# Kernel optimization log

Measured on AMD Instinct MI355X. Metric: run time of the kernel, lower is better.

Reference implementation:

```python
import jax, jax.numpy as jnp
import numpy as np

B, NV, RN, SN = 1, 4, 1024, 128
H = W = 256
C_FEAT = 32   # img_feat_dim
D_VIEW = 32   # view transformer d_model
PE_D = 8      # PE_d_hid
D_RAY = D_VIEW + PE_D  # 40
NHEAD = 8
EPS_LN = 1e-5


def _layernorm(x, g, b):
    m = x.mean(-1, keepdims=True)
    v = ((x - m) ** 2).mean(-1, keepdims=True)
    return (x - m) * jax.lax.rsqrt(v + EPS_LN) * g + b


def _linear_attention(q, k, v):
    # LoFTR kernelized linear attention; q,k,v: (n, L, h, d)
    Q = jax.nn.elu(q) + 1.0
    K = jax.nn.elu(k) + 1.0
    L = v.shape[1]
    KV = jnp.einsum('nshd,nshv->nhdv', K, v / L)
    Z = 1.0 / (jnp.einsum('nlhd,nhd->nlh', Q, K.sum(axis=1)) + 1e-6)
    return jnp.einsum('nlhd,nhdv,nlh->nlhv', Q, KV, Z) * L


def _loftr_self_layer(x, Wq, Wk, Wv, Wm, g1, b1, W1, W2, g2, b2):
    # LoFTREncoderLayer with self-attention (x is both query and source)
    n, L, d = x.shape
    dim = d // NHEAD
    q = (x @ Wq).reshape(n, L, NHEAD, dim)
    k = (x @ Wk).reshape(n, L, NHEAD, dim)
    v = (x @ Wv).reshape(n, L, NHEAD, dim)
    msg = _linear_attention(q, k, v).reshape(n, L, d) @ Wm
    msg = _layernorm(msg, g1, b1)
    msg = jax.nn.relu(jnp.concatenate([x, msg], -1) @ W1) @ W2
    msg = _layernorm(msg, g2, b2)
    return x + msg


def _grid_sample_2d(img, pix):
    # img: (N,C,H,W); pix: (N,RN,SN,2) in pixel coords.
    # bilinear, align_corners=True, zero padding; mask = in-bounds.
    N, C, Hh, Ww = img.shape
    x, y = pix[..., 0], pix[..., 1]
    mask = ((x >= 0) & (x <= Ww - 1) & (y >= 0) & (y <= Hh - 1)).astype(img.dtype)
    x0 = jnp.floor(x)
    y0 = jnp.floor(y)
    flat = img.reshape(N, C, Hh * Ww)

    def gather(ix, iy):
        valid = ((ix >= 0) & (ix < Ww) & (iy >= 0) & (iy < Hh)).astype(img.dtype)
        idx = (jnp.clip(iy, 0, Hh - 1) * Ww + jnp.clip(ix, 0, Ww - 1)).astype(jnp.int32)
        out = jnp.take_along_axis(flat, idx.reshape(N, 1, -1), axis=2)
        return out.reshape(N, C, ix.shape[1], ix.shape[2]) * valid[:, None]

    wx1 = x - x0
    wy1 = y - y0
    out = (gather(x0, y0) * ((1 - wx1) * (1 - wy1))[:, None]
           + gather(x0 + 1, y0) * (wx1 * (1 - wy1))[:, None]
           + gather(x0, y0 + 1) * ((1 - wx1) * wy1)[:, None]
           + gather(x0 + 1, y0 + 1) * (wx1 * wy1)[:, None])
    return out, mask


def _order_posenc(d_hid, n):
    pos = np.arange(n)[:, None].astype(np.float64)
    j = np.arange(d_hid)[None, :]
    tab = pos / np.power(10000.0, 2 * (j // 2) / d_hid)
    tab[:, 0::2] = np.sin(tab[:, 0::2])
    tab[:, 1::2] = np.cos(tab[:, 1::2])
    return jnp.asarray(tab, dtype=jnp.float32)


def _forward(point3D, source_imgs, source_imgs_feat, ref_pose_inv, source_poses_inv,
             source_poses, view_token,
             vt_Wq, vt_Wk, vt_Wv, vt_Wm, vt_g1, vt_b1, vt_W1, vt_W2, vt_g2, vt_b2,
             rt_Wq, rt_Wk, rt_Wv, rt_Wm, rt_g1, rt_b1, rt_W1, rt_W2, rt_g2, rt_b2,
             dm_W1, dm_b1, dm_W2, dm_b2, dm_W3, dm_b3,
             rw_W1, rw_b1, rw_W2, rw_b2, rw_W3, rw_b3):
    b, nv, _, h, w = source_imgs.shape
    _, rn, sn, _ = point3D.shape

    # relative viewing directions (B,NV,RN,SN,3)
    v1 = point3D - ref_pose_inv[:, None, None, :3, -1]
    v2 = point3D[:, None] - source_poses_inv[:, :, None, None, :3, -1]
    v1 = v1 / jnp.linalg.norm(v1, axis=-1, keepdims=True)
    v2 = v2 / jnp.linalg.norm(v2, axis=-1, keepdims=True)
    dir_relative = v1[:, None] - v2

    # project points into all source views: (B,NV,3,RN,SN)
    pts_h = jnp.concatenate([point3D, jnp.ones_like(point3D[..., :1])], -1)
    pip = jnp.einsum('bnij,brsj->bnirs', source_poses, pts_h)[:, :, :3]
    mask_valid_depth = (pip[:, :, 2] > 0).astype(point3D.dtype)
    pix = pip[:, :, :2] / pip[:, :, 2:3]
    grid = jnp.moveaxis(pix, 2, -1).reshape(b * nv, rn, sn, 2)

    feat_s, mask = _grid_sample_2d(source_imgs_feat.reshape(b * nv, -1, h, w), grid)
    rgb_s, _ = _grid_sample_2d(source_imgs.reshape(b * nv, -1, h, w), grid)
    mask = mask.reshape(b, nv, rn, sn) * mask_valid_depth

    # per-point multi-view tokens: (B*RN*SN, NV, C)
    x = feat_s.reshape(b, nv, -1, rn, sn).transpose(0, 3, 4, 1, 2).reshape(b * rn * sn, nv, -1)
    tok = jnp.broadcast_to(view_token, (x.shape[0], 1, view_token.shape[-1]))
    x = jnp.concatenate([tok, x], axis=1)  # prepend view token -> L = NV+1
    x = _loftr_self_layer(x, vt_Wq, vt_Wk, vt_Wv, vt_Wm, vt_g1, vt_b1, vt_W1, vt_W2, vt_g2, vt_b2)

    x1 = jnp.moveaxis(x, 1, 0)          # (NV+1, B*RN*SN, C)
    view_feature = x1[1:]
    x = x1[0].reshape(b * rn, sn, -1)   # token output per sample along ray

    pe = _order_posenc(PE_D, sn)        # (SN, 8)
    x = jnp.concatenate([x, jnp.broadcast_to(pe, (b * rn, sn, PE_D))], -1)
    x = _loftr_self_layer(x, rt_Wq, rt_Wk, rt_Wv, rt_Wm, rt_g1, rt_b1, rt_W1, rt_W2, rt_g2, rt_b2)

    hdm = jax.nn.relu(x @ dm_W1 + dm_b1)
    hdm = jax.nn.relu(hdm @ dm_W2 + dm_b2)
    srdf = hdm @ dm_W3 + dm_b3           # (B*RN, SN, 1)

    # radiance blending weights over views
    vf = view_feature.reshape(nv, b, rn, sn, -1).transpose(1, 2, 3, 0, 4)  # (B,RN,SN,NV,C)
    dr = dir_relative.transpose(0, 2, 3, 1, 4)                             # (B,RN,SN,NV,3)
    xw = jnp.concatenate([vf, dr], -1)
    xw = jax.nn.relu(xw @ rw_W1 + rw_b1)
    xw = jax.nn.relu(xw @ rw_W2 + rw_b2)
    xw = xw @ rw_W3 + rw_b3                                                # (B,RN,SN,NV,1)
    m = mask.transpose(0, 2, 3, 1)[..., None]
    xw = jnp.where(m == 0, -1e9, xw)
    weight = jax.nn.softmax(xw, axis=-2)
    w_bn = weight[..., 0].transpose(0, 3, 1, 2)[:, :, None]                # (B,NV,1,RN,SN)
    radiance = (rgb_s.reshape(b, nv, 3, rn, sn) * w_bn).sum(axis=1)        # (B,3,RN,SN)
    radiance = radiance.transpose(0, 2, 3, 1).reshape(b * rn * sn, 3)
    return radiance, srdf, pip


def setup_inputs() -> dict:
    key = jax.random.key(0)
    ks = jax.random.split(key, 4)
    u = jax.random.uniform(ks[0], (B, RN, SN, 3), dtype=jnp.float32)
    point3D = jnp.concatenate([u[..., :2] - 0.5, u[..., 2:] + 1.0], -1)  # x,y in [-.5,.5], z in [1,2]
    source_imgs = jax.random.normal(ks[1], (B, NV, 3, H, W), dtype=jnp.float32) * 0.5
    source_imgs_feat = jax.random.normal(ks[2], (B, NV, C_FEAT, H, W), dtype=jnp.float32) * 0.5

    f = 200.0
    P = np.array([[f, 0, W / 2, 0], [0, f, H / 2, 0], [0, 0, 1, 0], [0, 0, 0, 1]], np.float32)
    source_poses = jnp.asarray(np.broadcast_to(P, (B, NV, 4, 4)).copy())
    ref_pose_inv = jnp.asarray(np.broadcast_to(np.eye(4, dtype=np.float32), (B, 4, 4)).copy())
    spi = np.broadcast_to(np.eye(4, dtype=np.float32), (B, NV, 4, 4)).copy()
    spi[:, :, 0, 3] = np.linspace(-0.2, 0.2, NV, dtype=np.float32)  # camera centers
    source_poses_inv = jnp.asarray(spi)

    pk = jax.random.split(ks[3], 20)

    def lin(k, i, o):
        return jax.random.normal(k, (i, o), dtype=jnp.float32) * 0.05

    d, dr = D_VIEW, D_RAY
    params = dict(
        view_token=jax.random.normal(pk[0], (1, d), dtype=jnp.float32),
        vt_Wq=lin(pk[1], d, d), vt_Wk=lin(pk[2], d, d), vt_Wv=lin(pk[3], d, d), vt_Wm=lin(pk[4], d, d),
        vt_g1=jnp.ones(d), vt_b1=jnp.zeros(d),
        vt_W1=lin(pk[5], 2 * d, 2 * d), vt_W2=lin(pk[6], 2 * d, d),
        vt_g2=jnp.ones(d), vt_b2=jnp.zeros(d),
        rt_Wq=lin(pk[7], dr, dr), rt_Wk=lin(pk[8], dr, dr), rt_Wv=lin(pk[9], dr, dr), rt_Wm=lin(pk[10], dr, dr),
        rt_g1=jnp.ones(dr), rt_b1=jnp.zeros(dr),
        rt_W1=lin(pk[11], 2 * dr, 2 * dr), rt_W2=lin(pk[12], 2 * dr, dr),
        rt_g2=jnp.ones(dr), rt_b2=jnp.zeros(dr),
        dm_W1=lin(pk[13], dr, 32), dm_b1=jnp.zeros(32),
        dm_W2=lin(pk[14], 32, 16), dm_b2=jnp.zeros(16),
        dm_W3=lin(pk[15], 16, 1), dm_b3=jnp.zeros(1),
        rw_W1=lin(pk[16], d + 3, 16), rw_b1=jnp.zeros(16),
        rw_W2=lin(pk[17], 16, 8), rw_b2=jnp.zeros(8),
        rw_W3=lin(pk[18], 8, 1), rw_b3=jnp.zeros(1),
    )
    out = dict(point3D=point3D, source_imgs=source_imgs, source_imgs_feat=source_imgs_feat,
               ref_pose_inv=ref_pose_inv, source_poses_inv=source_poses_inv,
               source_poses=source_poses)
    out.update(params)
    return out


def reference(point3D, source_imgs, source_imgs_feat, ref_pose_inv, source_poses_inv,
              source_poses, view_token,
              vt_Wq, vt_Wk, vt_Wv, vt_Wm, vt_g1, vt_b1, vt_W1, vt_W2, vt_g2, vt_b2,
              rt_Wq, rt_Wk, rt_Wv, rt_Wm, rt_g1, rt_b1, rt_W1, rt_W2, rt_g2, rt_b2,
              dm_W1, dm_b1, dm_W2, dm_b2, dm_W3, dm_b3,
              rw_W1, rw_b1, rw_W2, rw_b2, rw_W3, rw_b3):
    return _forward(point3D, source_imgs, source_imgs_feat, ref_pose_inv, source_poses_inv,
                    source_poses, view_token,
                    vt_Wq, vt_Wk, vt_Wv, vt_Wm, vt_g1, vt_b1, vt_W1, vt_W2, vt_g2, vt_b2,
                    rt_Wq, rt_Wk, rt_Wv, rt_Wm, rt_g1, rt_b1, rt_W1, rt_W2, rt_g2, rt_b2,
                    dm_W1, dm_b1, dm_W2, dm_b2, dm_W3, dm_b3,
                    rw_W1, rw_b1, rw_W2, rw_b2, rw_W3, rw_b3)
```

## Files before the change

kernel.cpp:

```cpp
#include <hip/hip_runtime.h>
#include <math.h>

#define NPTS   131072
#define NVIEW  4
#define IMH    256
#define IMW    256

#define WS_FEATT   0u
#define WS_IMGT    8388608u
#define WS_X1      9437184u
#define WS_XR      26214400u
#define WS_MSG     31457280u
#define WS_RGB     36700160u
#define WS_DIR     38273024u
#define WS_MASK    39845888u

__device__ __forceinline__ float elup1(float t) { return t > 0.f ? t + 1.f : expf(t); }

__global__ __launch_bounds__(256) void k0_transpose(
    const float* __restrict__ feat, const float* __restrict__ img,
    float* __restrict__ featT, float* __restrict__ imgT)
{
    int tid = blockIdx.x * 256 + threadIdx.x;
    int v = tid >> 16, pix = tid & 65535;
    float buf[32];
#pragma unroll
    for (int c = 0; c < 32; ++c)
        buf[c] = feat[((size_t)(v * 32 + c) << 16) + pix];
    float4* dst = (float4*)(featT + ((size_t)tid << 5));
#pragma unroll
    for (int q = 0; q < 8; ++q)
        dst[q] = make_float4(buf[4*q], buf[4*q+1], buf[4*q+2], buf[4*q+3]);
    float4 rgb;
    rgb.x = img[((size_t)(v * 3 + 0) << 16) + pix];
    rgb.y = img[((size_t)(v * 3 + 1) << 16) + pix];
    rgb.z = img[((size_t)(v * 3 + 2) << 16) + pix];
    rgb.w = 0.f;
    *(float4*)(imgT + ((size_t)tid << 2)) = rgb;
}

__global__ __launch_bounds__(256) void k1_geom_sample(
    const float* __restrict__ p3d, const float* __restrict__ rpi,
    const float* __restrict__ spi, const float* __restrict__ sp,
    const float* __restrict__ featT, const float* __restrict__ imgT,
    float* __restrict__ x1, float* __restrict__ rgbw,
    float* __restrict__ dirw, float* __restrict__ maskw,
    float* __restrict__ outpip)
{
    int tid = blockIdx.x * 256 + threadIdx.x;
    int p = tid >> 2, v = tid & 3;
    float X = p3d[p * 3 + 0], Y = p3d[p * 3 + 1], Z = p3d[p * 3 + 2];

    float a0 = X - rpi[3], a1 = Y - rpi[7], a2 = Z - rpi[11];
    float na = sqrtf(a0 * a0 + a1 * a1 + a2 * a2);
    a0 /= na; a1 /= na; a2 /= na;
    const float* sv = spi + v * 16;
    float b0 = X - sv[3], b1 = Y - sv[7], b2 = Z - sv[11];
    float nb = sqrtf(b0 * b0 + b1 * b1 + b2 * b2);
    b0 /= nb; b1 /= nb; b2 /= nb;
    dirw[(size_t)p * 12 + v * 3 + 0] = a0 - b0;
    dirw[(size_t)p * 12 + v * 3 + 1] = a1 - b1;
    dirw[(size_t)p * 12 + v * 3 + 2] = a2 - b2;

    const float* P = sp + v * 16;
    float pip0 = P[0] * X + P[1] * Y + P[2]  * Z + P[3];
    float pip1 = P[4] * X + P[5] * Y + P[6]  * Z + P[7];
    float pip2 = P[8] * X + P[9] * Y + P[10] * Z + P[11];
    outpip[(size_t)(v * 3 + 0) * NPTS + p] = pip0;
    outpip[(size_t)(v * 3 + 1) * NPTS + p] = pip1;
    outpip[(size_t)(v * 3 + 2) * NPTS + p] = pip2;

    float gx = pip0 / pip2, gy = pip1 / pip2;
    float inb = (gx >= 0.f && gx <= 255.f && gy >= 0.f && gy <= 255.f) ? 1.f : 0.f;
    float mvd = pip2 > 0.f ? 1.f : 0.f;
    maskw[(size_t)p * 4 + v] = inb * mvd;

    float x0f = floorf(gx), y0f = floorf(gy);
    float wx = gx - x0f, wy = gy - y0f;
    int ix0 = (int)x0f, iy0 = (int)y0f;
    float tw[4] = { (1.f-wx)*(1.f-wy), wx*(1.f-wy), (1.f-wx)*wy, wx*wy };
    int tdx[4] = { 0, 1, 0, 1 };
    int tdy[4] = { 0, 0, 1, 1 };

    float facc[32];
#pragma unroll
    for (int c = 0; c < 32; ++c) facc[c] = 0.f;
    float r0 = 0.f, r1 = 0.f, r2 = 0.f;

#pragma unroll
    for (int tno = 0; tno < 4; ++tno) {
        int ix = ix0 + tdx[tno], iy = iy0 + tdy[tno];
        float valid = (ix >= 0 && ix < IMW && iy >= 0 && iy < IMH) ? 1.f : 0.f;
        int cx = min(max(ix, 0), IMW - 1), cy = min(max(iy, 0), IMH - 1);
        float wgt = tw[tno] * valid;
        size_t base = ((size_t)v << 16) + ((size_t)cy << 8) + (size_t)cx;
        const float4* fp = (const float4*)(featT + base * 32);
#pragma unroll
        for (int q = 0; q < 8; ++q) {
            float4 f4 = fp[q];
            facc[4*q+0] += f4.x * wgt; facc[4*q+1] += f4.y * wgt;
            facc[4*q+2] += f4.z * wgt; facc[4*q+3] += f4.w * wgt;
        }
        float4 rp = *(const float4*)(imgT + base * 4);
        r0 += rp.x * wgt; r1 += rp.y * wgt; r2 += rp.z * wgt;
    }

    float4* xd = (float4*)(x1 + ((size_t)p * 4 + v) * 32);
#pragma unroll
    for (int q = 0; q < 8; ++q)
        xd[q] = make_float4(facc[4*q], facc[4*q+1], facc[4*q+2], facc[4*q+3]);
    rgbw[(size_t)p * 12 + v * 3 + 0] = r0;
    rgbw[(size_t)p * 12 + v * 3 + 1] = r1;
    rgbw[(size_t)p * 12 + v * 3 + 2] = r2;
}

#define K2_BLK    128
#define K2_PTS    24
#define K2_GRID   1024
#define K2_NGRP   ((NPTS + K2_PTS - 1) / K2_PTS)

__device__ __forceinline__ void fma4(const float4 xv, const float* __restrict__ w,
                                     const int stride, float* __restrict__ acc)
{
#pragma unroll
    for (int j = 0; j < 32; ++j) acc[j] = fmaf(xv.x, w[j],            acc[j]);
#pragma unroll
    for (int j = 0; j < 32; ++j) acc[j] = fmaf(xv.y, w[stride + j],   acc[j]);
#pragma unroll
    for (int j = 0; j < 32; ++j) acc[j] = fmaf(xv.z, w[2*stride + j], acc[j]);
#pragma unroll
    for (int j = 0; j < 32; ++j) acc[j] = fmaf(xv.w, w[3*stride + j], acc[j]);
}

__device__ __forceinline__ void fma40(const float4 xv, const float* __restrict__ w,
                                      const int stride, float* __restrict__ acc)
{
#pragma unroll
    for (int j = 0; j < 40; ++j) acc[j] = fmaf(xv.x, w[j],            acc[j]);
#pragma unroll
    for (int j = 0; j < 40; ++j) acc[j] = fmaf(xv.y, w[stride + j],   acc[j]);
#pragma unroll
    for (int j = 0; j < 40; ++j) acc[j] = fmaf(xv.z, w[2*stride + j], acc[j]);
#pragma unroll
    for (int j = 0; j < 40; ++j) acc[j] = fmaf(xv.w, w[3*stride + j], acc[j]);
}

__global__ __launch_bounds__(K2_BLK) void k2_loftr1(
    float* __restrict__ x1g, const float* __restrict__ vtok,
    const float* __restrict__ Wq, const float* __restrict__ Wk,
    const float* __restrict__ Wv, const float* __restrict__ Wm,
    const float* __restrict__ g1v, const float* __restrict__ b1v,
    const float* __restrict__ W1, const float* __restrict__ W2,
    const float* __restrict__ g2v, const float* __restrict__ b2v,
    float* __restrict__ xr)
{
    __shared__ float shr[8192];

    int t = threadIdx.x;
    int pl = t / 5, l = t - pl * 5;
    bool act = (t < K2_PTS * 5);
    if (!act) { pl = 0; l = 0; }
    const int rowbase = (pl * 5 + l) * 68;

    for (int grp = blockIdx.x; grp < K2_NGRP; grp += gridDim.x) {
        int p = grp * K2_PTS + pl;
        bool valid = act && (p < NPTS);
        int pload = p < NPTS ? p : NPTS - 1;
        const float4* xsrc = (l == 0) ? (const float4*)vtok
                                      : (const float4*)(x1g + ((size_t)pload * 4 + (l - 1)) * 32);

        __syncthreads();

        {
            float acc[32];
#pragma unroll
            for (int j = 0; j < 32; ++j) acc[j] = 0.f;
            for (int g = 0; g < 8; ++g) {
                float4 xv = xsrc[g];
                fma4(xv, &Wk[g * 128], 32, acc);
            }
            if (act) {
                float* krow = &shr[rowbase];
#pragma unroll
                for (int j = 0; j < 32; j += 4)
                    *(float4*)&krow[j] = make_float4(elup1(acc[j]), elup1(acc[j+1]),
                                                     elup1(acc[j+2]), elup1(acc[j+3]));
            }
        }
        {
            float acc[32];
#pragma unroll
            for (int j = 0; j < 32; ++j) acc[j] = 0.f;
            for (int g = 0; g < 8; ++g) {
                float4 xv = xsrc[g];
                fma4(xv, &Wv[g * 128], 32, acc);
            }
            if (act) {
                float* vrow = &shr[rowbase + 32];
#pragma unroll
                for (int j = 0; j < 32; j += 4)
                    *(float4*)&vrow[j] = make_float4(acc[j], acc[j+1], acc[j+2], acc[j+3]);
            }
        }
        __syncthreads();

        float macc[32];
#pragma unroll
        for (int j = 0; j < 32; ++j) macc[j] = 0.f;
        for (int h = 0; h < 8; ++h) {
            float q0 = 0.f, q1 = 0.f, q2 = 0.f, q3 = 0.f;
            for (int g = 0; g < 8; ++g) {
                float4 xv = xsrc[g];
                const float* w = &Wq[g * 128 + h * 4];
                q0 = fmaf(xv.x, w[0],  q0); q1 = fmaf(xv.x, w[1],  q1);
                q2 = fmaf(xv.x, w[2],  q2); q3 = fmaf(xv.x, w[3],  q3);
                q0 = fmaf(xv.y, w[32], q0); q1 = fmaf(xv.y, w[33], q1);
                q2 = fmaf(xv.y, w[34], q2); q3 = fmaf(xv.y, w[35], q3);
                q0 = fmaf(xv.z, w[64], q0); q1 = fmaf(xv.z, w[65], q1);
                q2 = fmaf(xv.z, w[66], q2); q3 = fmaf(xv.z, w[67], q3);
                q0 = fmaf(xv.w, w[96], q0); q1 = fmaf(xv.w, w[97], q1);
                q2 = fmaf(xv.w, w[98], q2); q3 = fmaf(xv.w, w[99], q3);
            }
            q0 = elup1(q0); q1 = elup1(q1); q2 = elup1(q2); q3 = elup1(q3);

            float kvm[16] = {0,0,0,0,0,0,0,0,0,0,0,0,0,0,0,0};
            float ks0 = 0.f, ks1 = 0.f, ks2 = 0.f, ks3 = 0.f;
#pragma unroll
            for (int l2 = 0; l2 < 5; ++l2) {
                const float* row = &shr[(pl * 5 + l2) * 68 + h * 4];
                float4 K4 = *(const float4*)row;
                float4 V4 = *(const float4*)(row + 32);
                kvm[0]  = fmaf(K4.x, V4.x, kvm[0]);  kvm[1]  = fmaf(K4.x, V4.y, kvm[1]);
                kvm[2]  = fmaf(K4.x, V4.z, kvm[2]);  kvm[3]  = fmaf(K4.x, V4.w, kvm[3]);
                kvm[4]  = fmaf(K4.y, V4.x, kvm[4]);  kvm[5]  = fmaf(K4.y, V4.y, kvm[5]);
                kvm[6]  = fmaf(K4.y, V4.z, kvm[6]);  kvm[7]  = fmaf(K4.y, V4.w, kvm[7]);
                kvm[8]  = fmaf(K4.z, V4.x, kvm[8]);  kvm[9]  = fmaf(K4.z, V4.y, kvm[9]);
                kvm[10] = fmaf(K4.z, V4.z, kvm[10]); kvm[11] = fmaf(K4.z, V4.w, kvm[11]);
                kvm[12] = fmaf(K4.w, V4.x, kvm[12]); kvm[13] = fmaf(K4.w, V4.y, kvm[13]);
                kvm[14] = fmaf(K4.w, V4.z, kvm[14]); kvm[15] = fmaf(K4.w, V4.w, kvm[15]);
                ks0 += K4.x; ks1 += K4.y; ks2 += K4.z; ks3 += K4.w;
            }
            float den = 1e-6f + q0*ks0 + q1*ks1 + q2*ks2 + q3*ks3;
            float inv = 1.f / den;
            float o0 = (q0*kvm[0] + q1*kvm[4] + q2*kvm[8]  + q3*kvm[12]) * inv;
            float o1 = (q0*kvm[1] + q1*kvm[5] + q2*kvm[9]  + q3*kvm[13]) * inv;
            float o2 = (q0*kvm[2] + q1*kvm[6] + q2*kvm[10] + q3*kvm[14]) * inv;
            float o3 = (q0*kvm[3] + q1*kvm[7] + q2*kvm[11] + q3*kvm[15]) * inv;

            const float* wm = &Wm[h * 4 * 32];
#pragma unroll
            for (int j = 0; j < 32; ++j) macc[j] = fmaf(o0, wm[j],      macc[j]);
#pragma unroll
            for (int j = 0; j < 32; ++j) macc[j] = fmaf(o1, wm[32 + j], macc[j]);
#pragma unroll
            for (int j = 0; j < 32; ++j) macc[j] = fmaf(o2, wm[64 + j], macc[j]);
#pragma unroll
            for (int j = 0; j < 32; ++j) macc[j] = fmaf(o3, wm[96 + j], macc[j]);
        }

        float msg[32];
        {
            float s1 = 0.f, s2 = 0.f;
#pragma unroll
            for (int j = 0; j < 32; ++j) { s1 += macc[j]; s2 += macc[j] * macc[j]; }
            float m  = s1 * (1.f / 32.f);
            float va = s2 * (1.f / 32.f) - m * m;
            float rs = rsqrtf(va + 1e-5f);
#pragma unroll
            for (int j = 0; j < 32; ++j)
                msg[j] = (macc[j] - m) * rs * g1v[j] + b1v[j];
        }
        __syncthreads();

#pragma unroll
        for (int g = 0; g < 8; ++g)
            *(float4*)&shr[(g * K2_BLK + t) * 4] =
                make_float4(msg[4*g], msg[4*g+1], msg[4*g+2], msg[4*g+3]);

        float oacc[32];
#pragma unroll
        for (int j = 0; j < 32; ++j) oacc[j] = 0.f;
        for (int half = 0; half < 2; ++half) {
            const int j0 = half * 32;
            float hacc[32];
#pragma unroll
            for (int j = 0; j < 32; ++j) hacc[j] = 0.f;
            for (int g = 0; g < 8; ++g) {
                float4 xv = xsrc[g];
                fma4(xv, &W1[(g * 4) * 64 + j0], 64, hacc);
            }
            for (int g = 0; g < 8; ++g) {
                float4 mv = *(const float4*)&shr[(g * K2_BLK + t) * 4];
                fma4(mv, &W1[(32 + g * 4) * 64 + j0], 64, hacc);
            }
#pragma unroll
            for (int j = 0; j < 32; j += 4)
                *(float4*)&shr[4096 + ((j >> 2) * K2_BLK + t) * 4] =
                    make_float4(fmaxf(hacc[j], 0.f),   fmaxf(hacc[j+1], 0.f),
                                fmaxf(hacc[j+2], 0.f), fmaxf(hacc[j+3], 0.f));
            for (int g = 0; g < 8; ++g) {
                float4 hv = *(const float4*)&shr[4096 + (g * K2_BLK + t) * 4];
                fma4(hv, &W2[(j0 + g * 4) * 32], 32, oacc);
            }
        }

        {
            float s1 = 0.f, s2 = 0.f;
#pragma unroll
            for (int j = 0; j < 32; ++j) { s1 += oacc[j]; s2 += oacc[j] * oacc[j]; }
            float m  = s1 * (1.f / 32.f);
            float va = s2 * (1.f / 32.f) - m * m;
            float rs = rsqrtf(va + 1e-5f);

            if (valid) {
                float y[32];
#pragma unroll
                for (int g = 0; g < 8; ++g) {
                    float4 x4 = xsrc[g];
                    y[4*g] = x4.x; y[4*g+1] = x4.y; y[4*g+2] = x4.z; y[4*g+3] = x4.w;
                }
#pragma unroll
                for (int j = 0; j < 32; ++j)
                    y[j] += (oacc[j] - m) * rs * g2v[j] + b2v[j];

                if (l == 0) {
                    float4* dst = (float4*)(xr + (size_t)p * 40);
#pragma unroll
                    for (int g = 0; g < 8; ++g)
                        dst[g] = make_float4(y[4*g], y[4*g+1], y[4*g+2], y[4*g+3]);
                    int sidx = p & 127;
#pragma unroll
                    for (int c = 0; c < 8; ++c) {
                        float den = (c < 2) ? 1.f : (c < 4) ? 10.f : (c < 6) ? 100.f : 1000.f;
                        float arg = (float)sidx / den;
                        xr[(size_t)p * 40 + 32 + c] = (c & 1) ? cosf(arg) : sinf(arg);
                    }
                } else {
                    float4* dst = (float4*)(x1g + ((size_t)p * 4 + (l - 1)) * 32);
#pragma unroll
                    for (int g = 0; g < 8; ++g)
                        dst[g] = make_float4(y[4*g], y[4*g+1], y[4*g+2], y[4*g+3]);
                }
            }
        }
    }
}

#define KT_STRIDE 132
__global__ __launch_bounds__(128) void k3a_attn(
    const float* __restrict__ xr,
    const float* __restrict__ Wq, const float* __restrict__ Wk,
    const float* __restrict__ Wv, const float* __restrict__ Wm,
    const float* __restrict__ g1, const float* __restrict__ b1,
    float* __restrict__ msg)
{
    __shared__ float KT[40 * KT_STRIDE];
    __shared__ float VT[40 * KT_STRIDE];
    __shared__ float kvb[200];
    __shared__ float ksb[40];

    int t = threadIdx.x, r = blockIdx.x;
    const float4* x4 = (const float4*)(xr + ((size_t)r * 128 + t) * 40);

    {
        float acc[40];
#pragma unroll
        for (int j = 0; j < 40; ++j) acc[j] = 0.f;
        for (int g = 0; g < 10; ++g)
            fma40(x4[g], &Wk[g * 160], 40, acc);
#pragma unroll
        for (int j = 0; j < 40; ++j) KT[j * KT_STRIDE + t] = elup1(acc[j]);
    }
    {
        float acc[40];
#pragma unroll
        for (int j = 0; j < 40; ++j) acc[j] = 0.f;
        for (int g = 0; g < 10; ++g)
            fma40(x4[g], &Wv[g * 160], 40, acc);
#pragma unroll
        for (int j = 0; j < 40; ++j) VT[j * KT_STRIDE + t] = acc[j];
    }
    __syncthreads();

    {
        int lane = t & 63, wid = t >> 6;
        if (lane < 20) {
            int idx = wid * 20 + lane;
            int h = idx / 5;
            float ks = 0.f;
            float kv0 = 0.f, kv1 = 0.f, kv2 = 0.f, kv3 = 0.f, kv4 = 0.f;
            const float* kr = &KT[idx * KT_STRIDE];
            const float* v0 = &VT[(h * 5 + 0) * KT_STRIDE];
            const float* v1 = &VT[(h * 5 + 1) * KT_STRIDE];
            const float* v2 = &VT[(h * 5 + 2) * KT_STRIDE];
            const float* v3 = &VT[(h * 5 + 3) * KT_STRIDE];
            const float* v4 = &VT[(h * 5 + 4) * KT_STRIDE];
            for (int s = 0; s < 128; s += 4) {
                float4 K4 = *(const float4*)&kr[s];
                float4 A = *(const float4*)&v0[s];
                float4 B = *(const float4*)&v1[s];
                float4 C = *(const float4*)&v2[s];
                float4 D = *(const float4*)&v3[s];
                float4 E = *(const float4*)&v4[s];
                ks  += K4.x + K4.y + K4.z + K4.w;
                kv0 += K4.x*A.x + K4.y*A.y + K4.z*A.z + K4.w*A.w;
                kv1 += K4.x*B.x + K4.y*B.y + K4.z*B.z + K4.w*B.w;
                kv2 += K4.x*C.x + K4.y*C.y + K4.z*C.z + K4.w*C.w;
                kv3 += K4.x*D.x + K4.y*D.y + K4.z*D.z + K4.w*D.w;
                kv4 += K4.x*E.x + K4.y*E.y + K4.z*E.z + K4.w*E.w;
            }
            ksb[idx] = ks;
            kvb[idx * 5 + 0] = kv0; kvb[idx * 5 + 1] = kv1;
            kvb[idx * 5 + 2] = kv2; kvb[idx * 5 + 3] = kv3;
            kvb[idx * 5 + 4] = kv4;
        }
    }
    __syncthreads();

    float o[40];
    {
        float q[40];
#pragma unroll
        for (int j = 0; j < 40; ++j) q[j] = 0.f;
        for (int g = 0; g < 10; ++g)
            fma40(x4[g], &Wq[g * 160], 40, q);
#pragma unroll
        for (int j = 0; j < 40; ++j) q[j] = elup1(q[j]);

#pragma unroll
        for (int h = 0; h < 8; ++h) {
            float den = 1e-6f;
#pragma unroll
            for (int e = 0; e < 5; ++e) den += q[h*5+e] * ksb[h*5+e];
            float inv = 1.f / den;
#pragma unroll
            for (int d = 0; d < 5; ++d) {
                float val = 0.f;
#pragma unroll
                for (int e = 0; e < 5; ++e)
                    val += q[h*5+e] * kvb[(h*5+e)*5 + d];
                o[h*5+d] = val * inv;
            }
        }
    }
    float macc[40];
#pragma unroll
    for (int j = 0; j < 40; ++j) macc[j] = 0.f;
#pragma unroll
    for (int g = 0; g < 10; ++g) {
        float4 ov = make_float4(o[4*g], o[4*g+1], o[4*g+2], o[4*g+3]);
        fma40(ov, &Wm[g * 160], 40, macc);
    }
    {
        float s1 = 0.f, s2 = 0.f;
#pragma unroll
        for (int j = 0; j < 40; ++j) { s1 += macc[j]; s2 += macc[j] * macc[j]; }
        float mu = s1 * (1.f / 40.f);
        float va = s2 * (1.f / 40.f) - mu * mu;
        float rs = rsqrtf(va + 1e-5f);
#pragma unroll
        for (int j = 0; j < 40; ++j)
            macc[j] = (macc[j] - mu) * rs * g1[j] + b1[j];
    }
    float4* md = (float4*)(msg + ((size_t)r * 128 + t) * 40);
#pragma unroll
    for (int g = 0; g < 10; ++g)
        md[g] = make_float4(macc[4*g], macc[4*g+1], macc[4*g+2], macc[4*g+3]);
}

__global__ __launch_bounds__(128) void k3b_ffn(
    float* __restrict__ xr, const float* __restrict__ msg,
    const float* __restrict__ W1, const float* __restrict__ W2,
    const float* __restrict__ g2, const float* __restrict__ b2)
{
    int p = blockIdx.x * 128 + threadIdx.x;
    const float4* x4 = (const float4*)(xr + (size_t)p * 40);
    const float4* m4 = (const float4*)(msg + (size_t)p * 40);

    float oacc[40];
#pragma unroll
    for (int j = 0; j < 40; ++j) oacc[j] = 0.f;

#pragma unroll
    for (int half = 0; half < 2; ++half) {
        const int j0 = half * 40;
        float hacc[40];
#pragma unroll
        for (int j = 0; j < 40; ++j) hacc[j] = 0.f;
        for (int g = 0; g < 10; ++g)
            fma40(x4[g], &W1[(g * 4) * 80 + j0], 80, hacc);
        for (int g = 0; g < 10; ++g)
            fma40(m4[g], &W1[(40 + g * 4) * 80 + j0], 80, hacc);
#pragma unroll
        for (int j = 0; j < 40; ++j) hacc[j] = fmaxf(hacc[j], 0.f);
#pragma unroll
        for (int g = 0; g < 10; ++g) {
            float4 hv = make_float4(hacc[4*g], hacc[4*g+1], hacc[4*g+2], hacc[4*g+3]);
            fma40(hv, &W2[(j0 + g * 4) * 40], 40, oacc);
        }
    }

    float s1 = 0.f, s2 = 0.f;
#pragma unroll
    for (int j = 0; j < 40; ++j) { s1 += oacc[j]; s2 += oacc[j] * oacc[j]; }
    float mu = s1 * (1.f / 40.f);
    float va = s2 * (1.f / 40.f) - mu * mu;
    float rs = rsqrtf(va + 1e-5f);

    float4* dst = (float4*)(xr + (size_t)p * 40);
#pragma unroll
    for (int g = 0; g < 10; ++g) {
        float4 xv = x4[g];
        float4 o4;
        o4.x = xv.x + (oacc[4*g+0] - mu) * rs * g2[4*g+0] + b2[4*g+0];
        o4.y = xv.y + (oacc[4*g+1] - mu) * rs * g2[4*g+1] + b2[4*g+1];
        o4.z = xv.z + (oacc[4*g+2] - mu) * rs * g2[4*g+2] + b2[4*g+2];
        o4.w = xv.w + (oacc[4*g+3] - mu) * rs * g2[4*g+3] + b2[4*g+3];
        dst[g] = o4;
    }
}

__global__ __launch_bounds__(256) void k4_dm(
    const float* __restrict__ xr,
    const float* __restrict__ W1, const float* __restrict__ b1,
    const float* __restrict__ W2, const float* __restrict__ b2,
    const float* __restrict__ W3, const float* __restrict__ b3,
    float* __restrict__ out1)
{
    __shared__ float s[1857];
    int t = threadIdx.x;
    for (int i = t; i < 1280; i += 256) s[i] = W1[i];
    if (t < 32) s[1280 + t] = b1[t];
    for (int i = t; i < 512; i += 256) s[1312 + i] = W2[i];
    if (t < 16) { s[1824 + t] = b2[t]; s[1840 + t] = W3[t]; }
    if (t == 0) s[1856] = b3[0];
    __syncthreads();

    int p = blockIdx.x * 256 + t;
    float x[40];
    const float4* xp = (const float4*)(xr + (size_t)p * 40);
#pragma unroll
    for (int i = 0; i < 10; ++i) {
        float4 v4 = xp[i];
        x[4*i] = v4.x; x[4*i+1] = v4.y; x[4*i+2] = v4.z; x[4*i+3] = v4.w;
    }
    float h1[32];
#pragma unroll
    for (int j = 0; j < 32; ++j) h1[j] = s[1280 + j];
    for (int k = 0; k < 40; ++k) {
        float xv = x[k];
#pragma unroll
        for (int j = 0; j < 32; ++j) h1[j] += xv * s[k * 32 + j];
    }
#pragma unroll
    for (int j = 0; j < 32; ++j) h1[j] = fmaxf(h1[j], 0.f);
    float h2[16];
#pragma unroll
    for (int j = 0; j < 16; ++j) h2[j] = s[1824 + j];
    for (int k = 0; k < 32; ++k) {
        float hv = h1[k];
#pragma unroll
        for (int j = 0; j < 16; ++j) h2[j] += hv * s[1312 + k * 16 + j];
    }
    float o = s[1856];
#pragma unroll
    for (int j = 0; j < 16; ++j) o += fmaxf(h2[j], 0.f) * s[1840 + j];
    out1[p] = o;
}

__global__ __launch_bounds__(256) void k5_rw(
    const float* __restrict__ vf, const float* __restrict__ dirw,
    const float* __restrict__ maskw, const float* __restrict__ rgbw,
    const float* __restrict__ W1, const float* __restrict__ b1,
    const float* __restrict__ W2, const float* __restrict__ b2,
    const float* __restrict__ W3, const float* __restrict__ b3,
    float* __restrict__ out0)
{
    __shared__ float s[721];
    int t = threadIdx.x;
    for (int i = t; i < 560; i += 256) s[i] = W1[i];
    if (t < 16) s[560 + t] = b1[t];
    if (t < 128) s[576 + t] = W2[t];
    if (t < 8) { s[704 + t] = b2[t]; s[712 + t] = W3[t]; }
    if (t == 0) s[720] = b3[0];
    __syncthreads();

    int p = blockIdx.x * 256 + t;
    float xw[4];
#pragma unroll
    for (int v = 0; v < 4; ++v) {
        float in[35];
        const float4* vp = (const float4*)(vf + ((size_t)p * 4 + v) * 32);
#pragma unroll
        for (int q = 0; q < 8; ++q) {
            float4 f4 = vp[q];
            in[4*q] = f4.x; in[4*q+1] = f4.y; in[4*q+2] = f4.z; in[4*q+3] = f4.w;
        }
        in[32] = dirw[(size_t)p * 12 + v * 3 + 0];
        in[33] = dirw[(size_t)p * 12 + v * 3 + 1];
        in[34] = dirw[(size_t)p * 12 + v * 3 + 2];
        float h1[16];
#pragma unroll
        for (int j = 0; j < 16; ++j) h1[j] = s[560 + j];
        for (int k = 0; k < 35; ++k) {
            float xv = in[k];
#pragma unroll
            for (int j = 0; j < 16; ++j) h1[j] += xv * s[k * 16 + j];
        }
        float h2[8];
#pragma unroll
        for (int j = 0; j < 8; ++j) h2[j] = s[704 + j];
        for (int k = 0; k < 16; ++k) {
            float hv = fmaxf(h1[k], 0.f);
#pragma unroll
            for (int j = 0; j < 8; ++j) h2[j] += hv * s[576 + k * 8 + j];
        }
        float o = s[720];
#pragma unroll
        for (int j = 0; j < 8; ++j) o += fmaxf(h2[j], 0.f) * s[712 + j];
        xw[v] = (maskw[(size_t)p * 4 + v] == 0.f) ? -1e9f : o;
    }
    float m = fmaxf(fmaxf(xw[0], xw[1]), fmaxf(xw[2], xw[3]));
    float e0 = expf(xw[0] - m), e1 = expf(xw[1] - m), e2 = expf(xw[2] - m), e3 = expf(xw[3] - m);
    float inv = 1.f / (e0 + e1 + e2 + e3);
    float w4[4] = { e0 * inv, e1 * inv, e2 * inv, e3 * inv };
    float r0 = 0.f, r1 = 0.f, r2 = 0.f;
#pragma unroll
    for (int v = 0; v < 4; ++v) {
        r0 += rgbw[(size_t)p * 12 + v * 3 + 0] * w4[v];
        r1 += rgbw[(size_t)p * 12 + v * 3 + 1] * w4[v];
        r2 += rgbw[(size_t)p * 12 + v * 3 + 2] * w4[v];
    }
    out0[(size_t)p * 3 + 0] = r0;
    out0[(size_t)p * 3 + 1] = r1;
    out0[(size_t)p * 3 + 2] = r2;
}

extern "C" void kernel_launch(void* const* d_in, const int* in_sizes, int n_in,
                              void* d_out, int out_size, void* d_ws, size_t ws_size,
                              hipStream_t stream) {
    (void)in_sizes; (void)n_in; (void)out_size; (void)ws_size;
    const float* p3d   = (const float*)d_in[0];
    const float* imgs  = (const float*)d_in[1];
    const float* feat  = (const float*)d_in[2];
    const float* rpi   = (const float*)d_in[3];
    const float* spi   = (const float*)d_in[4];
    const float* sp    = (const float*)d_in[5];
    const float* vtok  = (const float*)d_in[6];
    const float* vtWq  = (const float*)d_in[7];
    const float* vtWk  = (const float*)d_in[8];
    const float* vtWv  = (const float*)d_in[9];
    const float* vtWm  = (const float*)d_in[10];
    const float* vtg1  = (const float*)d_in[11];
    const float* vtb1  = (const float*)d_in[12];
    const float* vtW1  = (const float*)d_in[13];
    const float* vtW2  = (const float*)d_in[14];
    const float* vtg2  = (const float*)d_in[15];
    const float* vtb2  = (const float*)d_in[16];
    const float* rtWq  = (const float*)d_in[17];
    const float* rtWk  = (const float*)d_in[18];
    const float* rtWv  = (const float*)d_in[19];
    const float* rtWm  = (const float*)d_in[20];
    const float* rtg1  = (const float*)d_in[21];
    const float* rtb1  = (const float*)d_in[22];
    const float* rtW1  = (const float*)d_in[23];
    const float* rtW2  = (const float*)d_in[24];
    const float* rtg2  = (const float*)d_in[25];
    const float* rtb2  = (const float*)d_in[26];
    const float* dmW1  = (const float*)d_in[27];
    const float* dmb1  = (const float*)d_in[28];
    const float* dmW2  = (const float*)d_in[29];
    const float* dmb2  = (const float*)d_in[30];
    const float* dmW3  = (const float*)d_in[31];
    const float* dmb3  = (const float*)d_in[32];
    const float* rwW1  = (const float*)d_in[33];
    const float* rwb1  = (const float*)d_in[34];
    const float* rwW2  = (const float*)d_in[35];
    const float* rwb2  = (const float*)d_in[36];
    const float* rwW3  = (const float*)d_in[37];
    const float* rwb3  = (const float*)d_in[38];

    float* out  = (float*)d_out;
    float* out0 = out;
    float* out1 = out + 393216;
    float* out2 = out + 524288;

    float* ws    = (float*)d_ws;
    float* featT = ws + WS_FEATT;
    float* imgT  = ws + WS_IMGT;
    float* x1    = ws + WS_X1;
    float* xr    = ws + WS_XR;
    float* msg   = ws + WS_MSG;
    float* rgbw  = ws + WS_RGB;
    float* dirw  = ws + WS_DIR;
    float* maskw = ws + WS_MASK;

    k0_transpose<<<dim3(1024), dim3(256), 0, stream>>>(feat, imgs, featT, imgT);
    k1_geom_sample<<<dim3(2048), dim3(256), 0, stream>>>(p3d, rpi, spi, sp, featT, imgT,
                                                         x1, rgbw, dirw, maskw, out2);
    k2_loftr1<<<dim3(K2_GRID), dim3(K2_BLK), 0, stream>>>(x1, vtok, vtWq, vtWk, vtWv, vtWm,
                                                    vtg1, vtb1, vtW1, vtW2, vtg2, vtb2, xr);
    k3a_attn<<<dim3(1024), dim3(128), 0, stream>>>(xr, rtWq, rtWk, rtWv, rtWm, rtg1, rtb1, msg);
    k3b_ffn<<<dim3(1024), dim3(128), 0, stream>>>(xr, msg, rtW1, rtW2, rtg2, rtb2);
    k4_dm<<<dim3(512), dim3(256), 0, stream>>>(xr, dmW1, dmb1, dmW2, dmb2, dmW3, dmb3, out1);
    k5_rw<<<dim3(512), dim3(256), 0, stream>>>(x1, dirw, maskw, rgbw,
                                               rwW1, rwb1, rwW2, rwb2, rwW3, rwb3, out0);
}
```

Baseline: 1.010 ms.

## Fuse ray attention, FFN and density MLP into one kernel; keep LoFTR1 FFN in registers

Merges the ray-transformer attention, FFN and density MLP kernels into one kernel, so the msg buffer and the intermediate xr no longer round-trip through global memory and two launches are removed. In the view-transformer kernel, Q is computed once for all heads instead of per head, and the FFN intermediates stay in registers instead of going through shared memory, splitting the hidden layer into quarters. The K2 grid grows and its shared buffer shrinks. The cost is higher register pressure, and the density MLP now reads weights from global/constant memory instead of LDS.

```diff
diff --git a/kernel.cpp b/kernel.cpp
--- a/kernel.cpp
+++ b/kernel.cpp
@@ -114,36 +114,62 @@
     rgbw[(size_t)p * 12 + v * 3 + 2] = r2;
 }
 
+__device__ __forceinline__ void fma4(const float4 xv, const float* __restrict__ w,
+                                     const int stride, float* __restrict__ acc)
+{
+#pragma unroll
+    for (int j = 0; j < 32; ++j) acc[j] = fmaf(xv.x, w[j],            acc[j]);
+#pragma unroll
+    for (int j = 0; j < 32; ++j) acc[j] = fmaf(xv.y, w[stride + j],   acc[j]);
+#pragma unroll
+    for (int j = 0; j < 32; ++j) acc[j] = fmaf(xv.z, w[2*stride + j], acc[j]);
+#pragma unroll
+    for (int j = 0; j < 32; ++j) acc[j] = fmaf(xv.w, w[3*stride + j], acc[j]);
+}
+
+__device__ __forceinline__ void fma16(const float4 xv, const float* __restrict__ w,
+                                      const int stride, float* __restrict__ acc)
+{
+#pragma unroll
+    for (int j = 0; j < 16; ++j) acc[j] = fmaf(xv.x, w[j],            acc[j]);
+#pragma unroll
+    for (int j = 0; j < 16; ++j) acc[j] = fmaf(xv.y, w[stride + j],   acc[j]);
+#pragma unroll
+    for (int j = 0; j < 16; ++j) acc[j] = fmaf(xv.z, w[2*stride + j], acc[j]);
+#pragma unroll
+    for (int j = 0; j < 16; ++j) acc[j] = fmaf(xv.w, w[3*stride + j], acc[j]);
+}
+
+__device__ __forceinline__ void fma40(const float4 xv, const float* __restrict__ w,
+                                      const int stride, float* __restrict__ acc)
+{
+#pragma unroll
+    for (int j = 0; j < 40; ++j) acc[j] = fmaf(xv.x, w[j],            acc[j]);
+#pragma unroll
+    for (int j = 0; j < 40; ++j) acc[j] = fmaf(xv.y, w[stride + j],   acc[j]);
+#pragma unroll
+    for (int j = 0; j < 40; ++j) acc[j] = fmaf(xv.z, w[2*stride + j], acc[j]);
+#pragma unroll
+    for (int j = 0; j < 40; ++j) acc[j] = fmaf(xv.w, w[3*stride + j], acc[j]);
+}
+
+__device__ __forceinline__ void fma20(const float4 xv, const float* __restrict__ w,
+                                      const int stride, float* __restrict__ acc)
+{
+#pragma unroll
+    for (int j = 0; j < 20; ++j) acc[j] = fmaf(xv.x, w[j],            acc[j]);
+#pragma unroll
+    for (int j = 0; j < 20; ++j) acc[j] = fmaf(xv.y, w[stride + j],   acc[j]);
+#pragma unroll
+    for (int j = 0; j < 20; ++j) acc[j] = fmaf(xv.z, w[2*stride + j], acc[j]);
+#pragma unroll
+    for (int j = 0; j < 20; ++j) acc[j] = fmaf(xv.w, w[3*stride + j], acc[j]);
+}
+
 #define K2_BLK    128
 #define K2_PTS    24
-#define K2_GRID   1024
+#define K2_GRID   1280
 #define K2_NGRP   ((NPTS + K2_PTS - 1) / K2_PTS)
-
-__device__ __forceinline__ void fma4(const float4 xv, const float* __restrict__ w,
-                                     const int stride, float* __restrict__ acc)
-{
-#pragma unroll
-    for (int j = 0; j < 32; ++j) acc[j] = fmaf(xv.x, w[j],            acc[j]);
-#pragma unroll
-    for (int j = 0; j < 32; ++j) acc[j] = fmaf(xv.y, w[stride + j],   acc[j]);
-#pragma unroll
-    for (int j = 0; j < 32; ++j) acc[j] = fmaf(xv.z, w[2*stride + j], acc[j]);
-#pragma unroll
-    for (int j = 0; j < 32; ++j) acc[j] = fmaf(xv.w, w[3*stride + j], acc[j]);
-}
-
-__device__ __forceinline__ void fma40(const float4 xv, const float* __restrict__ w,
-                                      const int stride, float* __restrict__ acc)
-{
-#pragma unroll
-    for (int j = 0; j < 40; ++j) acc[j] = fmaf(xv.x, w[j],            acc[j]);
-#pragma unroll
-    for (int j = 0; j < 40; ++j) acc[j] = fmaf(xv.y, w[stride + j],   acc[j]);
-#pragma unroll
-    for (int j = 0; j < 40; ++j) acc[j] = fmaf(xv.z, w[2*stride + j], acc[j]);
-#pragma unroll
-    for (int j = 0; j < 40; ++j) acc[j] = fmaf(xv.w, w[3*stride + j], acc[j]);
-}
 
 __global__ __launch_bounds__(K2_BLK) void k2_loftr1(
     float* __restrict__ x1g, const float* __restrict__ vtok,
@@ -154,7 +180,7 @@
     const float* __restrict__ g2v, const float* __restrict__ b2v,
     float* __restrict__ xr)
 {
-    __shared__ float shr[8192];
+    __shared__ float shr[K2_PTS * 5 * 68];
 
     int t = threadIdx.x;
     int pl = t / 5, l = t - pl * 5;
@@ -204,24 +230,23 @@
         }
         __syncthreads();
 
+        float q[32];
+        {
+#pragma unroll
+            for (int j = 0; j < 32; ++j) q[j] = 0.f;
+            for (int g = 0; g < 8; ++g) {
+                float4 xv = xsrc[g];
+                fma4(xv, &Wq[g * 128], 32, q);
+            }
+#pragma unroll
+            for (int j = 0; j < 32; ++j) q[j] = elup1(q[j]);
+        }
+
         float macc[32];
 #pragma unroll
         for (int j = 0; j < 32; ++j) macc[j] = 0.f;
         for (int h = 0; h < 8; ++h) {
-            float q0 = 0.f, q1 = 0.f, q2 = 0.f, q3 = 0.f;
-            for (int g = 0; g < 8; ++g) {
-                float4 xv = xsrc[g];
-                const float* w = &Wq[g * 128 + h * 4];
-                q0 = fmaf(xv.x, w[0],  q0); q1 = fmaf(xv.x, w[1],  q1);
-                q2 = fmaf(xv.x, w[2],  q2); q3 = fmaf(xv.x, w[3],  q3);
-                q0 = fmaf(xv.y, w[32], q0); q1 = fmaf(xv.y, w[33], q1);
-                q2 = fmaf(xv.y, w[34], q2); q3 = fmaf(xv.y, w[35], q3);
-                q0 = fmaf(xv.z, w[64], q0); q1 = fmaf(xv.z, w[65], q1);
-                q2 = fmaf(xv.z, w[66], q2); q3 = fmaf(xv.z, w[67], q3);
-                q0 = fmaf(xv.w, w[96], q0); q1 = fmaf(xv.w, w[97], q1);
-                q2 = fmaf(xv.w, w[98], q2); q3 = fmaf(xv.w, w[99], q3);
-            }
-            q0 = elup1(q0); q1 = elup1(q1); q2 = elup1(q2); q3 = elup1(q3);
+            float q0 = q[h*4+0], q1 = q[h*4+1], q2 = q[h*4+2], q3 = q[h*4+3];
 
             float kvm[16] = {0,0,0,0,0,0,0,0,0,0,0,0,0,0,0,0};
             float ks0 = 0.f, ks1 = 0.f, ks2 = 0.f, ks3 = 0.f;
@@ -258,7 +283,6 @@
             for (int j = 0; j < 32; ++j) macc[j] = fmaf(o3, wm[96 + j], macc[j]);
         }
 
-        float msg[32];
         {
             float s1 = 0.f, s2 = 0.f;
 #pragma unroll
@@ -268,39 +292,33 @@
             float rs = rsqrtf(va + 1e-5f);
 #pragma unroll
             for (int j = 0; j < 32; ++j)
-                msg[j] = (macc[j] - m) * rs * g1v[j] + b1v[j];
-        }
-        __syncthreads();
-
-#pragma unroll
-        for (int g = 0; g < 8; ++g)
-            *(float4*)&shr[(g * K2_BLK + t) * 4] =
-                make_float4(msg[4*g], msg[4*g+1], msg[4*g+2], msg[4*g+3]);
+                macc[j] = (macc[j] - m) * rs * g1v[j] + b1v[j];
+        }
 
         float oacc[32];
 #pragma unroll
         for (int j = 0; j < 32; ++j) oacc[j] = 0.f;
-        for (int half = 0; half < 2; ++half) {
-            const int j0 = half * 32;
-            float hacc[32];
-#pragma unroll
-            for (int j = 0; j < 32; ++j) hacc[j] = 0.f;
+#pragma unroll
+        for (int qq = 0; qq < 4; ++qq) {
+            const int j0 = qq * 16;
+            float hacc[16];
+#pragma unroll
+            for (int j = 0; j < 16; ++j) hacc[j] = 0.f;
             for (int g = 0; g < 8; ++g) {
                 float4 xv = xsrc[g];
-                fma4(xv, &W1[(g * 4) * 64 + j0], 64, hacc);
-            }
+                fma16(xv, &W1[(g * 4) * 64 + j0], 64, hacc);
+            }
+#pragma unroll
             for (int g = 0; g < 8; ++g) {
-                float4 mv = *(const float4*)&shr[(g * K2_BLK + t) * 4];
-                fma4(mv, &W1[(32 + g * 4) * 64 + j0], 64, hacc);
-            }
-#pragma unroll
-            for (int j = 0; j < 32; j += 4)
-                *(float4*)&shr[4096 + ((j >> 2) * K2_BLK + t) * 4] =
-                    make_float4(fmaxf(hacc[j], 0.f),   fmaxf(hacc[j+1], 0.f),
-                                fmaxf(hacc[j+2], 0.f), fmaxf(hacc[j+3], 0.f));
-            for (int g = 0; g < 8; ++g) {
-                float4 hv = *(const float4*)&shr[4096 + (g * K2_BLK + t) * 4];
-                fma4(hv, &W2[(j0 + g * 4) * 32], 32, oacc);
+                float4 mv = make_float4(macc[4*g], macc[4*g+1], macc[4*g+2], macc[4*g+3]);
+                fma16(mv, &W1[(32 + g * 4) * 64 + j0], 64, hacc);
+            }
+#pragma unroll
+            for (int j = 0; j < 16; ++j) hacc[j] = fmaxf(hacc[j], 0.f);
+#pragma unroll
+            for (int u = 0; u < 4; ++u) {
+                float4 hv = make_float4(hacc[4*u], hacc[4*u+1], hacc[4*u+2], hacc[4*u+3]);
+                fma4(hv, &W2[(j0 + u * 4) * 32], 32, oacc);
             }
         }
 
@@ -313,21 +331,19 @@
             float rs = rsqrtf(va + 1e-5f);
 
             if (valid) {
-                float y[32];
+                float4* dst = (l == 0) ? (float4*)(xr + (size_t)p * 40)
+                                       : (float4*)(x1g + ((size_t)p * 4 + (l - 1)) * 32);
 #pragma unroll
                 for (int g = 0; g < 8; ++g) {
                     float4 x4 = xsrc[g];
-                    y[4*g] = x4.x; y[4*g+1] = x4.y; y[4*g+2] = x4.z; y[4*g+3] = x4.w;
+                    float4 o4;
+                    o4.x = x4.x + (oacc[4*g+0] - m) * rs * g2v[4*g+0] + b2v[4*g+0];
+                    o4.y = x4.y + (oacc[4*g+1] - m) * rs * g2v[4*g+1] + b2v[4*g+1];
+                    o4.z = x4.z + (oacc[4*g+2] - m) * rs * g2v[4*g+2] + b2v[4*g+2];
+                    o4.w = x4.w + (oacc[4*g+3] - m) * rs * g2v[4*g+3] + b2v[4*g+3];
+                    dst[g] = o4;
                 }
-#pragma unroll
-                for (int j = 0; j < 32; ++j)
-                    y[j] += (oacc[j] - m) * rs * g2v[j] + b2v[j];
-
                 if (l == 0) {
-                    float4* dst = (float4*)(xr + (size_t)p * 40);
-#pragma unroll
-                    for (int g = 0; g < 8; ++g)
-                        dst[g] = make_float4(y[4*g], y[4*g+1], y[4*g+2], y[4*g+3]);
                     int sidx = p & 127;
 #pragma unroll
                     for (int c = 0; c < 8; ++c) {
@@ -335,11 +351,6 @@
                         float arg = (float)sidx / den;
                         xr[(size_t)p * 40 + 32 + c] = (c & 1) ? cosf(arg) : sinf(arg);
                     }
-                } else {
-                    float4* dst = (float4*)(x1g + ((size_t)p * 4 + (l - 1)) * 32);
-#pragma unroll
-                    for (int g = 0; g < 8; ++g)
-                        dst[g] = make_float4(y[4*g], y[4*g+1], y[4*g+2], y[4*g+3]);
                 }
             }
         }
@@ -347,12 +358,17 @@
 }
 
 #define KT_STRIDE 132
-__global__ __launch_bounds__(128) void k3a_attn(
+__global__ __launch_bounds__(128) void k3_fused(
     const float* __restrict__ xr,
     const float* __restrict__ Wq, const float* __restrict__ Wk,
     const float* __restrict__ Wv, const float* __restrict__ Wm,
     const float* __restrict__ g1, const float* __restrict__ b1,
-    float* __restrict__ msg)
+    const float* __restrict__ W1, const float* __restrict__ W2,
+    const float* __restrict__ g2, const float* __restrict__ b2,
+    const float* __restrict__ dmW1, const float* __restrict__ dmb1,
+    const float* __restrict__ dmW2, const float* __restrict__ dmb2,
+    const float* __restrict__ dmW3, const float* __restrict__ dmb3,
+    float* __restrict__ out1)
 {
     __shared__ float KT[40 * KT_STRIDE];
     __shared__ float VT[40 * KT_STRIDE];
@@ -462,110 +478,72 @@
         for (int j = 0; j < 40; ++j)
             macc[j] = (macc[j] - mu) * rs * g1[j] + b1[j];
     }
-    float4* md = (float4*)(msg + ((size_t)r * 128 + t) * 40);
-#pragma unroll
-    for (int g = 0; g < 10; ++g)
-        md[g] = make_float4(macc[4*g], macc[4*g+1], macc[4*g+2], macc[4*g+3]);
-}
-
-__global__ __launch_bounds__(128) void k3b_ffn(
-    float* __restrict__ xr, const float* __restrict__ msg,
-    const float* __restrict__ W1, const float* __restrict__ W2,
-    const float* __restrict__ g2, const float* __restrict__ b2)
-{
-    int p = blockIdx.x * 128 + threadIdx.x;
-    const float4* x4 = (const float4*)(xr + (size_t)p * 40);
-    const float4* m4 = (const float4*)(msg + (size_t)p * 40);
 
     float oacc[40];
 #pragma unroll
     for (int j = 0; j < 40; ++j) oacc[j] = 0.f;
-
-#pragma unroll
-    for (int half = 0; half < 2; ++half) {
-        const int j0 = half * 40;
-        float hacc[40];
-#pragma unroll
-        for (int j = 0; j < 40; ++j) hacc[j] = 0.f;
+#pragma unroll
+    for (int qq = 0; qq < 4; ++qq) {
+        const int j0 = qq * 20;
+        float hacc[20];
+#pragma unroll
+        for (int j = 0; j < 20; ++j) hacc[j] = 0.f;
         for (int g = 0; g < 10; ++g)
-            fma40(x4[g], &W1[(g * 4) * 80 + j0], 80, hacc);
-        for (int g = 0; g < 10; ++g)
-            fma40(m4[g], &W1[(40 + g * 4) * 80 + j0], 80, hacc);
-#pragma unroll
-        for (int j = 0; j < 40; ++j) hacc[j] = fmaxf(hacc[j], 0.f);
+            fma20(x4[g], &W1[(g * 4) * 80 + j0], 80, hacc);
 #pragma unroll
         for (int g = 0; g < 10; ++g) {
-            float4 hv = make_float4(hacc[4*g], hacc[4*g+1], hacc[4*g+2], hacc[4*g+3]);
-            fma40(hv, &W2[(j0 + g * 4) * 40], 40, oacc);
-        }
-    }
-
-    float s1 = 0.f, s2 = 0.f;
-#pragma unroll
-    for (int j = 0; j < 40; ++j) { s1 += oacc[j]; s2 += oacc[j] * oacc[j]; }
-    float mu = s1 * (1.f / 40.f);
-    float va = s2 * (1.f / 40.f) - mu * mu;
-    float rs = rsqrtf(va + 1e-5f);
-
-    float4* dst = (float4*)(xr + (size_t)p * 40);
-#pragma unroll
-    for (int g = 0; g < 10; ++g) {
-        float4 xv = x4[g];
-        float4 o4;
-        o4.x = xv.x + (oacc[4*g+0] - mu) * rs * g2[4*g+0] + b2[4*g+0];
-        o4.y = xv.y + (oacc[4*g+1] - mu) * rs * g2[4*g+1] + b2[4*g+1];
-        o4.z = xv.z + (oacc[4*g+2] - mu) * rs * g2[4*g+2] + b2[4*g+2];
-        o4.w = xv.w + (oacc[4*g+3] - mu) * rs * g2[4*g+3] + b2[4*g+3];
-        dst[g] = o4;
-    }
-}
-
-__global__ __launch_bounds__(256) void k4_dm(
-    const float* __restrict__ xr,
-    const float* __restrict__ W1, const float* __restrict__ b1,
-    const float* __restrict__ W2, const float* __restrict__ b2,
-    const float* __restrict__ W3, const float* __restrict__ b3,
-    float* __restrict__ out1)
-{
-    __shared__ float s[1857];
-    int t = threadIdx.x;
-    for (int i = t; i < 1280; i += 256) s[i] = W1[i];
-    if (t < 32) s[1280 + t] = b1[t];
-    for (int i = t; i < 512; i += 256) s[1312 + i] = W2[i];
-    if (t < 16) { s[1824 + t] = b2[t]; s[1840 + t] = W3[t]; }
-    if (t == 0) s[1856] = b3[0];
-    __syncthreads();
-
-    int p = blockIdx.x * 256 + t;
-    float x[40];
-    const float4* xp = (const float4*)(xr + (size_t)p * 40);
-#pragma unroll
-    for (int i = 0; i < 10; ++i) {
-        float4 v4 = xp[i];
-        x[4*i] = v4.x; x[4*i+1] = v4.y; x[4*i+2] = v4.z; x[4*i+3] = v4.w;
-    }
+            float4 mv = make_float4(macc[4*g], macc[4*g+1], macc[4*g+2], macc[4*g+3]);
+            fma20(mv, &W1[(40 + g * 4) * 80 + j0], 80, hacc);
+        }
+#pragma unroll
+        for (int j = 0; j < 20; ++j) hacc[j] = fmaxf(hacc[j], 0.f);
+#pragma unroll
+        for (int u = 0; u < 5; ++u) {
+            float4 hv = make_float4(hacc[4*u], hacc[4*u+1], hacc[4*u+2], hacc[4*u+3]);
+            fma40(hv, &W2[(j0 + u * 4) * 40], 40, oacc);
+        }
+    }
+
+    float y[40];
+    {
+        float s1 = 0.f, s2 = 0.f;
+#pragma unroll
+        for (int j = 0; j < 40; ++j) { s1 += oacc[j]; s2 += oacc[j] * oacc[j]; }
+        float mu = s1 * (1.f / 40.f);
+        float va = s2 * (1.f / 40.f) - mu * mu;
+        float rs = rsqrtf(va + 1e-5f);
+#pragma unroll
+        for (int g = 0; g < 10; ++g) {
+            float4 xv = x4[g];
+            y[4*g+0] = xv.x + (oacc[4*g+0] - mu) * rs * g2[4*g+0] + b2[4*g+0];
+            y[4*g+1] = xv.y + (oacc[4*g+1] - mu) * rs * g2[4*g+1] + b2[4*g+1];
+            y[4*g+2] = xv.z + (oacc[4*g+2] - mu) * rs * g2[4*g+2] + b2[4*g+2];
+            y[4*g+3] = xv.w + (oacc[4*g+3] - mu) * rs * g2[4*g+3] + b2[4*g+3];
+        }
+    }
+
     float h1[32];
 #pragma unroll
-    for (int j = 0; j < 32; ++j) h1[j] = s[1280 + j];
+    for (int j = 0; j < 32; ++j) h1[j] = dmb1[j];
     for (int k = 0; k < 40; ++k) {
-        float xv = x[k];
-#pragma unroll
-        for (int j = 0; j < 32; ++j) h1[j] += xv * s[k * 32 + j];
+        float yv = y[k];
+#pragma unroll
+        for (int j = 0; j < 32; ++j) h1[j] = fmaf(yv, dmW1[k * 32 + j], h1[j]);
     }
 #pragma unroll
     for (int j = 0; j < 32; ++j) h1[j] = fmaxf(h1[j], 0.f);
     float h2[16];
 #pragma unroll
-    for (int j = 0; j < 16; ++j) h2[j] = s[1824 + j];
+    for (int j = 0; j < 16; ++j) h2[j] = dmb2[j];
     for (int k = 0; k < 32; ++k) {
         float hv = h1[k];
 #pragma unroll
-        for (int j = 0; j < 16; ++j) h2[j] += hv * s[1312 + k * 16 + j];
-    }
-    float o = s[1856];
-#pragma unroll
-    for (int j = 0; j < 16; ++j) o += fmaxf(h2[j], 0.f) * s[1840 + j];
-    out1[p] = o;
+        for (int j = 0; j < 16; ++j) h2[j] = fmaf(hv, dmW2[k * 16 + j], h2[j]);
+    }
+    float oo = dmb3[0];
+#pragma unroll
+    for (int j = 0; j < 16; ++j) oo = fmaf(fmaxf(h2[j], 0.f), dmW3[j], oo);
+    out1[(size_t)r * 128 + t] = oo;
 }
 
 __global__ __launch_bounds__(256) void k5_rw(
@@ -690,7 +668,6 @@
     float* imgT  = ws + WS_IMGT;
     float* x1    = ws + WS_X1;
     float* xr    = ws + WS_XR;
-    float* msg   = ws + WS_MSG;
     float* rgbw  = ws + WS_RGB;
     float* dirw  = ws + WS_DIR;
     float* maskw = ws + WS_MASK;
@@ -700,9 +677,9 @@
                                                          x1, rgbw, dirw, maskw, out2);
     k2_loftr1<<<dim3(K2_GRID), dim3(K2_BLK), 0, stream>>>(x1, vtok, vtWq, vtWk, vtWv, vtWm,
                                                     vtg1, vtb1, vtW1, vtW2, vtg2, vtb2, xr);
-    k3a_attn<<<dim3(1024), dim3(128), 0, stream>>>(xr, rtWq, rtWk, rtWv, rtWm, rtg1, rtb1, msg);
-    k3b_ffn<<<dim3(1024), dim3(128), 0, stream>>>(xr, msg, rtW1, rtW2, rtg2, rtb2);
-    k4_dm<<<dim3(512), dim3(256), 0, stream>>>(xr, dmW1, dmb1, dmW2, dmb2, dmW3, dmb3, out1);
+    k3_fused<<<dim3(1024), dim3(128), 0, stream>>>(xr, rtWq, rtWk, rtWv, rtWm, rtg1, rtb1,
+                                                   rtW1, rtW2, rtg2, rtb2,
+                                                   dmW1, dmb1, dmW2, dmb2, dmW3, dmb3, out1);
     k5_rw<<<dim3(512), dim3(256), 0, stream>>>(x1, dirw, maskw, rgbw,
                                                rwW1, rwb1, rwW2, rwb2, rwW3, rwb3, out0);
 }
```

After: 2.648 ms. 162% more time.
